# Optimization experiments

Hardware: AMD Instinct MI355X
Metric: run time of the kernel (lower is better)

The kernel has to match this reference:

```python
import jax, jax.numpy as jnp
import numpy as np

MAX_PATCH = 40   # static pad >= max points per grid cell + 1 (grid/fake token slot)
NUM_HEADS = 8


def _cumcount_1d(cell):
    """For each element, number of earlier elements with the same cell id. O(U log U) via stable sort."""
    U = cell.shape[0]
    order = jnp.argsort(cell)              # stable
    sc = cell[order]
    pos = jnp.arange(U)
    new_run = jnp.concatenate([jnp.ones((1,), bool), sc[1:] != sc[:-1]])
    run_start = jax.lax.associative_scan(jnp.maximum, jnp.where(new_run, pos, 0))  # cummax
    return jnp.zeros(U, jnp.int32).at[order].set((pos - run_start).astype(jnp.int32))


def setup_inputs() -> dict:
    key = jax.random.key(0)
    ks = jax.random.split(key, 10)
    B, U, E = 8, 8192, 256
    n = m = 32
    coords = jnp.linspace(0.0, 1.0, n)
    grid = jnp.stack(jnp.meshgrid(coords, coords, indexing='ij'), axis=-1)  # [n,m,2]
    xc_on_grid = jnp.broadcast_to(grid, (B, n, m, 2))
    xc_off_grid = jax.random.uniform(ks[0], (B, U, 2))
    zc_off_grid = jax.random.normal(ks[1], (B, U, E), jnp.float32)
    zc_on_grid = jax.random.normal(ks[2], (B, n, m, E), jnp.float32)
    latents = jax.random.normal(ks[3], (n, m, E), jnp.float32)
    fake_embedding = jax.random.normal(ks[4], (E,), jnp.float32)
    sc = 1.0 / np.sqrt(E)
    Wq = jax.random.normal(ks[5], (E, E), jnp.float32) * sc
    Wk = jax.random.normal(ks[6], (E, E), jnp.float32) * sc
    Wv = jax.random.normal(ks[7], (E, E), jnp.float32) * sc
    Wo = jax.random.normal(ks[8], (E, E), jnp.float32) * sc
    return dict(xc_off_grid=xc_off_grid, xc_on_grid=xc_on_grid,
                zc_off_grid=zc_off_grid, zc_on_grid=zc_on_grid,
                latents=latents, fake_embedding=fake_embedding,
                Wq=Wq, Wk=Wk, Wv=Wv, Wo=Wo, ignore_on_grid=0)


def reference(xc_off_grid, xc_on_grid, zc_off_grid, zc_on_grid,
              latents, fake_embedding, Wq, Wk, Wv, Wo, ignore_on_grid):
    B, U, E = zc_off_grid.shape
    _, n, m, _ = xc_on_grid.shape
    S = n * m
    MP = MAX_PATCH

    # nearest grid cell per off-grid point (uniform grid on [0,1], n points/dim)
    row = jnp.clip(jnp.round(xc_off_grid[..., 0] * (n - 1)).astype(jnp.int32), 0, n - 1)
    col = jnp.clip(jnp.round(xc_off_grid[..., 1] * (m - 1)).astype(jnp.int32), 0, m - 1)
    cell = row * m + col                                    # [B,U]

    cumcount = jax.vmap(_cumcount_1d)(cell)                 # [B,U]
    counts = jnp.zeros((B, S), jnp.int32).at[jnp.arange(B)[:, None], cell].add(1)

    # scatter off-grid tokens into padded per-cell buckets [B*S, MP, E]
    bs = (jnp.arange(B)[:, None] * S + cell).reshape(-1)
    slot = jnp.where(cumcount < MP - 1, cumcount, MP).reshape(-1)  # overflow -> dropped
    gs = jnp.zeros((B * S, MP, E), zc_off_grid.dtype)
    gs = gs.at[bs, slot].set(zc_off_grid.reshape(B * U, E), mode='drop')

    # last slot: on-grid token (or fake embedding when ignore_on_grid)
    if ignore_on_grid:
        last = jnp.broadcast_to(fake_embedding, (B * S, E))
    else:
        last = zc_on_grid.reshape(B * S, E)
    gs = gs.at[:, MP - 1].set(last)

    slots = jnp.arange(MP)
    valid = (slots[None, :] < counts.reshape(-1)[:, None]) | (slots == MP - 1)  # [B*S, MP]

    # masked MHCA: one latent query per cell attends over its bucket
    H = NUM_HEADS
    hd = E // H
    lat = jnp.broadcast_to(latents.reshape(1, S, E), (B, S, E)).reshape(B * S, E)
    q = (lat @ Wq).reshape(B * S, H, hd)
    k = (gs @ Wk).reshape(B * S, MP, H, hd)
    v = (gs @ Wv).reshape(B * S, MP, H, hd)
    scores = jnp.einsum('bhd,bphd->bhp', q, k) / np.sqrt(hd)
    scores = jnp.where(valid[:, None, :], scores, -jnp.inf)
    attn = jax.nn.softmax(scores, axis=-1)
    out = jnp.einsum('bhp,bphd->bhd', attn, v).reshape(B * S, E) @ Wo
    z_grid = out.reshape(B, n, m, E)
    return (xc_on_grid, z_grid)
```

## Files before the change

kernel.cpp:

```cpp
#include <hip/hip_runtime.h>
#include <hip/hip_bf16.h>

#define B_   8
#define U_   8192
#define E_   256
#define N_   32
#define S_   1024
#define MP_  40
#define H_   8
#define NLIST 39
#define NCAP  35
#define NTOKMAX 36
#define GCELLS (B_*S_)
#define KDIM  (H_*E_)

typedef unsigned short ushort_t;
using bf16x8 = __attribute__((ext_vector_type(8))) short;
using f32x4  = __attribute__((ext_vector_type(4))) float;

#define WS_COUNTS 0u
#define WS_LISTS  32768u
#define WS_LATB   1310720u
#define WS_WQKT   1835008u
#define WS_WVOT   2883584u
#define WS_QKB    3932160u
#define WS_W      8126464u

__device__ inline unsigned pk2(float a, float b) {
    __hip_bfloat16 x = __float2bfloat16(a), y = __float2bfloat16(b);
    return ((unsigned)(*(ushort_t*)&y) << 16) | (unsigned)(*(ushort_t*)&x);
}
__device__ inline float ubf(ushort_t u) {
    unsigned v = (unsigned)u << 16;
    return *(float*)&v;
}

__global__ __launch_bounds__(256)
void prologue(const float* __restrict__ xc_on, float* __restrict__ out,
              int* __restrict__ counts) {
    int i = blockIdx.x * 256 + threadIdx.x;
    ((float4*)out)[i] = ((const float4*)xc_on)[i];
    if (i < 2048) ((int4*)counts)[i] = make_int4(0, 0, 0, 0);
}

__global__ __launch_bounds__(256)
void mega_prep(const float* __restrict__ xc_off, const float* __restrict__ latents,
               const float* __restrict__ Wq, const float* __restrict__ Wk,
               const float* __restrict__ Wv, const float* __restrict__ Wo,
               int* __restrict__ counts, int* __restrict__ lists,
               ushort_t* __restrict__ latb, ushort_t* __restrict__ wqkT,
               ushort_t* __restrict__ wvoT) {
    __shared__ float smem[10496];
    int blk = blockIdx.x, tid = threadIdx.x;

    if (blk < 256) {
        int t = blk * 256 + tid;
        float x = xc_off[2 * t], y = xc_off[2 * t + 1];
        int row = (int)rintf(x * 31.f); row = min(max(row, 0), 31);
        int col = (int)rintf(y * 31.f); col = min(max(col, 0), 31);
        int b = t >> 13;
        int g = b * S_ + row * N_ + col;
        int old = atomicAdd(&counts[g], 1);
        if (old < NLIST) lists[g * NLIST + old] = t & (U_ - 1);
    } else if (blk < 384) {
        int i = (blk - 256) * 256 + tid;
        const float4* src = (const float4*)latents + 2 * i;
        float4 a = src[0], c = src[1];
        uint4 o;
        o.x = pk2(a.x, a.y); o.y = pk2(a.z, a.w);
        o.z = pk2(c.x, c.y); o.w = pk2(c.z, c.w);
        ((uint4*)latb)[i] = o;
    } else if (blk < 448) {
        int b2 = blk - 384, h = b2 >> 3, e0 = (b2 & 7) * 32;
        float* wq_s = smem;
        for (int i = tid; i < 8192; i += 256) {
            int f = i >> 5, d = i & 31;
            wq_s[f * 33 + d] = Wq[f * E_ + h * 32 + d];
        }
        __syncthreads();
        int e = e0 + (tid & 31), fg = tid >> 5;
        float wk[32];
        #pragma unroll
        for (int d4 = 0; d4 < 8; ++d4) {
            float4 v = *(const float4*)(Wk + (size_t)e * E_ + h * 32 + d4 * 4);
            wk[d4*4] = v.x; wk[d4*4+1] = v.y; wk[d4*4+2] = v.z; wk[d4*4+3] = v.w;
        }
        const float invs = 0.17677669529663687f;
        ushort_t* dst = wqkT + (size_t)(h * E_ + e) * E_ + fg * 32;
        for (int q8 = 0; q8 < 4; ++q8) {
            float t8[8];
            #pragma unroll
            for (int k = 0; k < 8; ++k) {
                int f = fg * 32 + q8 * 8 + k;
                float acc = 0.f;
                #pragma unroll
                for (int d = 0; d < 32; ++d) acc += wq_s[f * 33 + d] * wk[d];
                t8[k] = acc * invs;
            }
            uint4 o;
            o.x = pk2(t8[0], t8[1]); o.y = pk2(t8[2], t8[3]);
            o.z = pk2(t8[4], t8[5]); o.w = pk2(t8[6], t8[7]);
            *(uint4*)(dst + q8 * 8) = o;
        }
    } else {
        int b3 = blk - 448, h = b3 >> 2, e0p = (b3 & 3) * 64;
        float* wv_s = smem;
        float* wo_s = smem + 8448;
        for (int i = tid; i < 8192; i += 256) {
            int e = i >> 5, d = i & 31;
            wv_s[e * 33 + d] = Wv[e * E_ + h * 32 + d];
        }
        for (int i = tid; i < 2048; i += 256) {
            int d = i >> 6, el = i & 63;
            wo_s[i] = Wo[(h * 32 + d) * E_ + e0p + el];
        }
        __syncthreads();
        int erow = tid & 63, eg = tid >> 6;
        float wor[32];
        #pragma unroll
        for (int d = 0; d < 32; ++d) wor[d] = wo_s[d * 64 + erow];
        ushort_t* dst = wvoT + (size_t)(e0p + erow) * KDIM + h * E_ + eg * 64;
        for (int q8 = 0; q8 < 8; ++q8) {
            float t8[8];
            #pragma unroll
            for (int k = 0; k < 8; ++k) {
                int e = eg * 64 + q8 * 8 + k;
                float acc = 0.f;
                #pragma unroll
                for (int d = 0; d < 32; ++d) acc += wv_s[e * 33 + d] * wor[d];
                t8[k] = acc;
            }
            uint4 o;
            o.x = pk2(t8[0], t8[1]); o.y = pk2(t8[2], t8[3]);
            o.z = pk2(t8[4], t8[5]); o.w = pk2(t8[6], t8[7]);
            *(uint4*)(dst + q8 * 8) = o;
        }
    }
}

template<bool BF16OUT>
__global__ __launch_bounds__(256)
void gemm_k(const ushort_t* __restrict__ A, const ushort_t* __restrict__ BT,
            void* __restrict__ Cv, int Kdim, int Ndim, int lgNTX) {
    constexpr int LDB = 72;
    __shared__ ushort_t As[64 * LDB];
    __shared__ ushort_t Bs[64 * LDB];
    int tid = threadIdx.x;
    int idx = blockIdx.x;
    idx = (idx & 7) * (gridDim.x >> 3) + (idx >> 3);
    int nTX = 1 << lgNTX;
    int m0 = (idx >> lgNTX) * 64, n0 = (idx & (nTX - 1)) * 64;

    int wave = tid >> 6, lane = tid & 63;
    int wr = wave >> 1, wc = wave & 1;
    int l15 = lane & 15, lg = lane >> 4;

    f32x4 acc[2][2];
    #pragma unroll
    for (int m = 0; m < 2; ++m)
        #pragma unroll
        for (int n = 0; n < 2; ++n)
            acc[m][n] = (f32x4){0.f, 0.f, 0.f, 0.f};

    int r0 = tid >> 3, u0 = tid & 7;
    int r1 = r0 + 32, u1 = u0;

    const ushort_t* pa0 = A  + (size_t)(m0 + r0) * Kdim + u0 * 8;
    const ushort_t* pa1 = A  + (size_t)(m0 + r1) * Kdim + u1 * 8;
    const ushort_t* pb0 = BT + (size_t)(n0 + r0) * Kdim + u0 * 8;
    const ushort_t* pb1 = BT + (size_t)(n0 + r1) * Kdim + u1 * 8;

    uint4 a0 = *(const uint4*)(pa0);
    uint4 a1 = *(const uint4*)(pa1);
    uint4 b0 = *(const uint4*)(pb0);
    uint4 b1 = *(const uint4*)(pb1);

    for (int kt = 0; kt < Kdim; kt += 64) {
        __syncthreads();
        *(uint4*)(As + r0 * LDB + u0 * 8) = a0;
        *(uint4*)(As + r1 * LDB + u1 * 8) = a1;
        *(uint4*)(Bs + r0 * LDB + u0 * 8) = b0;
        *(uint4*)(Bs + r1 * LDB + u1 * 8) = b1;
        __syncthreads();
        if (kt + 64 < Kdim) {
            a0 = *(const uint4*)(pa0 + kt + 64);
            a1 = *(const uint4*)(pa1 + kt + 64);
            b0 = *(const uint4*)(pb0 + kt + 64);
            b1 = *(const uint4*)(pb1 + kt + 64);
        }
        #pragma unroll
        for (int kk = 0; kk < 2; ++kk) {
            bf16x8 af[2], bfr[2];
            #pragma unroll
            for (int m = 0; m < 2; ++m)
                af[m] = *(const bf16x8*)(As + (wr * 32 + m * 16 + l15) * LDB + (kk * 4 + lg) * 8);
            #pragma unroll
            for (int n = 0; n < 2; ++n)
                bfr[n] = *(const bf16x8*)(Bs + (wc * 32 + n * 16 + l15) * LDB + (kk * 4 + lg) * 8);
            #pragma unroll
            for (int m = 0; m < 2; ++m)
                #pragma unroll
                for (int n = 0; n < 2; ++n)
                    acc[m][n] = __builtin_amdgcn_mfma_f32_16x16x32_bf16(
                        af[m], bfr[n], acc[m][n], 0, 0, 0);
        }
    }
    #pragma unroll
    for (int m = 0; m < 2; ++m)
        #pragma unroll
        for (int n = 0; n < 2; ++n)
            #pragma unroll
            for (int q = 0; q < 4; ++q) {
                int row = m0 + wr * 32 + m * 16 + lg * 4 + q;
                int col = n0 + wc * 32 + n * 16 + l15;
                if (BF16OUT) {
                    __hip_bfloat16 hb = __float2bfloat16(acc[m][n][q]);
                    ((ushort_t*)Cv)[(size_t)row * Ndim + col] = *(ushort_t*)&hb;
                } else {
                    ((float*)Cv)[(size_t)row * Ndim + col] = acc[m][n][q];
                }
            }
}

__global__ __launch_bounds__(256, 8)
void pool_cells(const float* __restrict__ zc_off, const float* __restrict__ zc_on,
                const float* __restrict__ fake, const ushort_t* __restrict__ qkb,
                const int* __restrict__ counts, const int* __restrict__ lists,
                const int* __restrict__ ig_p, ushort_t* __restrict__ wout) {
    __shared__ __align__(16) ushort_t tok[NTOKMAX * E_];
    __shared__ float sc[H_ * 48];

    int g = blockIdx.x, s = g & (S_ - 1), b = g >> 10, tid = threadIdx.x;
    int h = tid >> 5, j = tid & 31;

    int cnt = min(counts[g], NCAP);
    int ntok = cnt + 1, ig = ig_p[0];
    const float* lastrow = ig ? fake : zc_on + (size_t)g * E_;

    {
        uint4* t4 = (uint4*)tok;
        for (int i = tid; i < ntok * 32; i += 256) {
            int p = i >> 5, q = i & 31;
            const float* src = (p < cnt)
                ? zc_off + ((size_t)b * U_ + lists[g * NLIST + p]) * E_
                : lastrow;
            float4 x = *(const float4*)(src + q * 8);
            float4 y = *(const float4*)(src + q * 8 + 4);
            uint4 o;
            o.x = pk2(x.x, x.y); o.y = pk2(x.z, x.w);
            o.z = pk2(y.x, y.y); o.w = pk2(y.z, y.w);
            t4[((p << 5) + q) ^ (p & 7)] = o;
        }
    }
    __syncthreads();

    if (tid < 64) {
        int l15 = tid & 15, lg = tid >> 4;
        bf16x8 af[8];
        const ushort_t* qrow = qkb + (size_t)s * KDIM + l15 * E_ + lg * 8;
        #pragma unroll
        for (int kk = 0; kk < 8; ++kk)
            af[kk] = *(const bf16x8*)(qrow + kk * 32);
        const bf16x8* tv = (const bf16x8*)tok;
        int ntiles = (ntok + 15) >> 4;
        for (int t = 0; t < ntiles; ++t) {
            f32x4 acc = (f32x4){0.f, 0.f, 0.f, 0.f};
            int row = t * 16 + l15;
            int rc = row < NTOKMAX ? row : NTOKMAX - 1;
            #pragma unroll
            for (int kk = 0; kk < 8; ++kk) {
                bf16x8 bfr = tv[((rc << 5) + (kk << 2) + lg) ^ (rc & 7)];
                acc = __builtin_amdgcn_mfma_f32_16x16x32_bf16(af[kk], bfr, acc, 0, 0, 0);
            }
            if (lg < 2) {
                #pragma unroll
                for (int q = 0; q < 4; ++q)
                    sc[(lg * 4 + q) * 48 + t * 16 + l15] = acc[q];
            }
        }
    }
    __syncthreads();

    {
        float v0 = (j < ntok) ? sc[h * 48 + j] : -1e30f;
        float v1 = (j + 32 < ntok) ? sc[h * 48 + j + 32] : -1e30f;
        float mx = fmaxf(v0, v1);
        #pragma unroll
        for (int off = 16; off; off >>= 1) mx = fmaxf(mx, __shfl_xor(mx, off, 32));
        float e0 = (j < ntok) ? __expf(v0 - mx) : 0.f;
        float e1 = (j + 32 < ntok) ? __expf(v1 - mx) : 0.f;
        float sm = e0 + e1;
        #pragma unroll
        for (int off = 16; off; off >>= 1) sm += __shfl_xor(sm, off, 32);
        float inv = 1.f / sm;
        if (j < ntok)      sc[h * 48 + j] = e0 * inv;
        if (j + 32 < ntok) sc[h * 48 + j + 32] = e1 * inv;
    }

    float acc[8];
    #pragma unroll
    for (int k = 0; k < 8; ++k) acc[k] = 0.f;
    const bf16x8* tv2 = (const bf16x8*)tok;
    for (int p = 0; p < ntok; ++p) {
        float a = sc[h * 48 + p];
        bf16x8 t8 = tv2[((p << 5) + j) ^ (p & 7)];
        #pragma unroll
        for (int k = 0; k < 8; ++k) acc[k] += a * ubf((ushort_t)t8[k]);
    }
    uint4 o;
    o.x = pk2(acc[0], acc[1]); o.y = pk2(acc[2], acc[3]);
    o.z = pk2(acc[4], acc[5]); o.w = pk2(acc[6], acc[7]);
    ((uint4*)(wout + (size_t)g * KDIM))[tid] = o;
}

extern "C" void kernel_launch(void* const* d_in, const int* in_sizes, int n_in,
                              void* d_out, int out_size, void* d_ws, size_t ws_size,
                              hipStream_t stream) {
    const float* xc_off  = (const float*)d_in[0];
    const float* xc_on   = (const float*)d_in[1];
    const float* zc_off  = (const float*)d_in[2];
    const float* zc_on   = (const float*)d_in[3];
    const float* latents = (const float*)d_in[4];
    const float* fake    = (const float*)d_in[5];
    const float* Wq      = (const float*)d_in[6];
    const float* Wk      = (const float*)d_in[7];
    const float* Wv      = (const float*)d_in[8];
    const float* Wo      = (const float*)d_in[9];
    const int*   ig      = (const int*)d_in[10];
    float* out = (float*)d_out;

    char* ws = (char*)d_ws;
    int*      counts = (int*)(ws + WS_COUNTS);
    int*      lists  = (int*)(ws + WS_LISTS);
    ushort_t* latb   = (ushort_t*)(ws + WS_LATB);
    ushort_t* wqkT   = (ushort_t*)(ws + WS_WQKT);
    ushort_t* wvoT   = (ushort_t*)(ws + WS_WVOT);
    ushort_t* qkb    = (ushort_t*)(ws + WS_QKB);
    ushort_t* w      = (ushort_t*)(ws + WS_W);

    const int PASS = B_ * N_ * N_ * 2;

    prologue<<<16, 256, 0, stream>>>(xc_on, out, counts);

    mega_prep<<<480, 256, 0, stream>>>(xc_off, latents, Wq, Wk, Wv, Wo,
                                       counts, lists, latb, wqkT, wvoT);

    gemm_k<true><<<512, 256, 0, stream>>>(latb, wqkT, qkb, 256, KDIM, 5);

    pool_cells<<<GCELLS, 256, 0, stream>>>(zc_off, zc_on, fake, qkb,
                                           counts, lists, ig, w);

    gemm_k<false><<<512, 256, 0, stream>>>(w, wvoT, out + PASS, KDIM, E_, 2);
}
```

Measured before the change: 83.57 us.

## Merge prologue into prep, fold bucket build into first GEMM, widen K tile

```diff
diff --git a/kernel.cpp b/kernel.cpp
--- a/kernel.cpp
+++ b/kernel.cpp
@@ -13,6 +13,7 @@
 #define NTOKMAX 36
 #define GCELLS (B_*S_)
 #define KDIM  (H_*E_)
+#define GEMMBLK 512
 
 typedef unsigned short ushort_t;
 using bf16x8 = __attribute__((ext_vector_type(8))) short;
@@ -36,25 +37,104 @@
 }
 
 __global__ __launch_bounds__(256)
-void prologue(const float* __restrict__ xc_on, float* __restrict__ out,
-              int* __restrict__ counts) {
-    int i = blockIdx.x * 256 + threadIdx.x;
-    ((float4*)out)[i] = ((const float4*)xc_on)[i];
-    if (i < 2048) ((int4*)counts)[i] = make_int4(0, 0, 0, 0);
-}
-
-__global__ __launch_bounds__(256)
-void mega_prep(const float* __restrict__ xc_off, const float* __restrict__ latents,
-               const float* __restrict__ Wq, const float* __restrict__ Wk,
-               const float* __restrict__ Wv, const float* __restrict__ Wo,
-               int* __restrict__ counts, int* __restrict__ lists,
-               ushort_t* __restrict__ latb, ushort_t* __restrict__ wqkT,
-               ushort_t* __restrict__ wvoT) {
+void prep(const float* __restrict__ latents,
+          const float* __restrict__ Wq, const float* __restrict__ Wk,
+          const float* __restrict__ Wv, const float* __restrict__ Wo,
+          const float* __restrict__ xc_on, float* __restrict__ out,
+          int* __restrict__ counts,
+          ushort_t* __restrict__ latb, ushort_t* __restrict__ wqkT,
+          ushort_t* __restrict__ wvoT) {
     __shared__ float smem[10496];
     int blk = blockIdx.x, tid = threadIdx.x;
 
-    if (blk < 256) {
-        int t = blk * 256 + tid;
+    if (blk < 128) {
+        int i = blk * 256 + tid;
+        const float4* src = (const float4*)latents + 2 * i;
+        float4 a = src[0], c = src[1];
+        uint4 o;
+        o.x = pk2(a.x, a.y); o.y = pk2(a.z, a.w);
+        o.z = pk2(c.x, c.y); o.w = pk2(c.z, c.w);
+        ((uint4*)latb)[i] = o;
+    } else if (blk < 192) {
+        int b2 = blk - 128, h = b2 >> 3, e0 = (b2 & 7) * 32;
+        float* wq_s = smem;
+        for (int i = tid; i < 8192; i += 256) {
+            int f = i >> 5, d = i & 31;
+            wq_s[f * 33 + d] = Wq[f * E_ + h * 32 + d];
+        }
+        __syncthreads();
+        int e = e0 + (tid & 31), fg = tid >> 5;
+        float wk[32];
+        #pragma unroll
+        for (int d4 = 0; d4 < 8; ++d4) {
+            float4 v = *(const float4*)(Wk + (size_t)e * E_ + h * 32 + d4 * 4);
+            wk[d4*4] = v.x; wk[d4*4+1] = v.y; wk[d4*4+2] = v.z; wk[d4*4+3] = v.w;
+        }
+        const float invs = 0.17677669529663687f;
+        ushort_t* dst = wqkT + (size_t)(h * E_ + e) * E_ + fg * 32;
+        for (int q8 = 0; q8 < 4; ++q8) {
+            float t8[8];
+            #pragma unroll
+            for (int k = 0; k < 8; ++k) {
+                int f = fg * 32 + q8 * 8 + k;
+                float acc = 0.f;
+                #pragma unroll
+                for (int d = 0; d < 32; ++d) acc += wq_s[f * 33 + d] * wk[d];
+                t8[k] = acc * invs;
+            }
+            uint4 o;
+            o.x = pk2(t8[0], t8[1]); o.y = pk2(t8[2], t8[3]);
+            o.z = pk2(t8[4], t8[5]); o.w = pk2(t8[6], t8[7]);
+            *(uint4*)(dst + q8 * 8) = o;
+        }
+    } else if (blk < 224) {
+        int b3 = blk - 192, h = b3 >> 2, e0p = (b3 & 3) * 64;
+        float* wv_s = smem;
+        float* wo_s = smem + 8448;
+        for (int i = tid; i < 8192; i += 256) {
+            int e = i >> 5, d = i & 31;
+            wv_s[e * 33 + d] = Wv[e * E_ + h * 32 + d];
+        }
+        for (int i = tid; i < 2048; i += 256) {
+            int d = i >> 6, el = i & 63;
+            wo_s[i] = Wo[(h * 32 + d) * E_ + e0p + el];
+        }
+        __syncthreads();
+        int erow = tid & 63, eg = tid >> 6;
+        float wor[32];
+        #pragma unroll
+        for (int d = 0; d < 32; ++d) wor[d] = wo_s[d * 64 + erow];
+        ushort_t* dst = wvoT + (size_t)(e0p + erow) * KDIM + h * E_ + eg * 64;
+        for (int q8 = 0; q8 < 8; ++q8) {
+            float t8[8];
+            #pragma unroll
+            for (int k = 0; k < 8; ++k) {
+                int e = eg * 64 + q8 * 8 + k;
+                float acc = 0.f;
+                #pragma unroll
+                for (int d = 0; d < 32; ++d) acc += wv_s[e * 33 + d] * wor[d];
+                t8[k] = acc;
+            }
+            uint4 o;
+            o.x = pk2(t8[0], t8[1]); o.y = pk2(t8[2], t8[3]);
+            o.z = pk2(t8[4], t8[5]); o.w = pk2(t8[6], t8[7]);
+            *(uint4*)(dst + q8 * 8) = o;
+        }
+    } else {
+        int i = (blk - 224) * 256 + tid;
+        ((float4*)out)[i] = ((const float4*)xc_on)[i];
+        if (i < 2048) ((int4*)counts)[i] = make_int4(0, 0, 0, 0);
+    }
+}
+
+template<int BKT, bool BF16OUT, bool DO_BUILD>
+__global__ __launch_bounds__(256)
+void gemm_k(const ushort_t* __restrict__ A, const ushort_t* __restrict__ BT,
+            void* __restrict__ Cv, int Kdim, int Ndim, int lgNTX,
+            const float* __restrict__ xc_off, int* __restrict__ counts,
+            int* __restrict__ lists) {
+    if (DO_BUILD && (int)blockIdx.x >= GEMMBLK) {
+        int t = ((int)blockIdx.x - GEMMBLK) * 256 + threadIdx.x;
         float x = xc_off[2 * t], y = xc_off[2 * t + 1];
         int row = (int)rintf(x * 31.f); row = min(max(row, 0), 31);
         int col = (int)rintf(y * 31.f); col = min(max(col, 0), 31);
@@ -62,92 +142,16 @@
         int g = b * S_ + row * N_ + col;
         int old = atomicAdd(&counts[g], 1);
         if (old < NLIST) lists[g * NLIST + old] = t & (U_ - 1);
-    } else if (blk < 384) {
-        int i = (blk - 256) * 256 + tid;
-        const float4* src = (const float4*)latents + 2 * i;
-        float4 a = src[0], c = src[1];
-        uint4 o;
-        o.x = pk2(a.x, a.y); o.y = pk2(a.z, a.w);
-        o.z = pk2(c.x, c.y); o.w = pk2(c.z, c.w);
-        ((uint4*)latb)[i] = o;
-    } else if (blk < 448) {
-        int b2 = blk - 384, h = b2 >> 3, e0 = (b2 & 7) * 32;
-        float* wq_s = smem;
-        for (int i = tid; i < 8192; i += 256) {
-            int f = i >> 5, d = i & 31;
-            wq_s[f * 33 + d] = Wq[f * E_ + h * 32 + d];
-        }
-        __syncthreads();
-        int e = e0 + (tid & 31), fg = tid >> 5;
-        float wk[32];
-        #pragma unroll
-        for (int d4 = 0; d4 < 8; ++d4) {
-            float4 v = *(const float4*)(Wk + (size_t)e * E_ + h * 32 + d4 * 4);
-            wk[d4*4] = v.x; wk[d4*4+1] = v.y; wk[d4*4+2] = v.z; wk[d4*4+3] = v.w;
-        }
-        const float invs = 0.17677669529663687f;
-        ushort_t* dst = wqkT + (size_t)(h * E_ + e) * E_ + fg * 32;
-        for (int q8 = 0; q8 < 4; ++q8) {
-            float t8[8];
-            #pragma unroll
-            for (int k = 0; k < 8; ++k) {
-                int f = fg * 32 + q8 * 8 + k;
-                float acc = 0.f;
-                #pragma unroll
-                for (int d = 0; d < 32; ++d) acc += wq_s[f * 33 + d] * wk[d];
-                t8[k] = acc * invs;
-            }
-            uint4 o;
-            o.x = pk2(t8[0], t8[1]); o.y = pk2(t8[2], t8[3]);
-            o.z = pk2(t8[4], t8[5]); o.w = pk2(t8[6], t8[7]);
-            *(uint4*)(dst + q8 * 8) = o;
-        }
-    } else {
-        int b3 = blk - 448, h = b3 >> 2, e0p = (b3 & 3) * 64;
-        float* wv_s = smem;
-        float* wo_s = smem + 8448;
-        for (int i = tid; i < 8192; i += 256) {
-            int e = i >> 5, d = i & 31;
-            wv_s[e * 33 + d] = Wv[e * E_ + h * 32 + d];
-        }
-        for (int i = tid; i < 2048; i += 256) {
-            int d = i >> 6, el = i & 63;
-            wo_s[i] = Wo[(h * 32 + d) * E_ + e0p + el];
-        }
-        __syncthreads();
-        int erow = tid & 63, eg = tid >> 6;
-        float wor[32];
-        #pragma unroll
-        for (int d = 0; d < 32; ++d) wor[d] = wo_s[d * 64 + erow];
-        ushort_t* dst = wvoT + (size_t)(e0p + erow) * KDIM + h * E_ + eg * 64;
-        for (int q8 = 0; q8 < 8; ++q8) {
-            float t8[8];
-            #pragma unroll
-            for (int k = 0; k < 8; ++k) {
-                int e = eg * 64 + q8 * 8 + k;
-                float acc = 0.f;
-                #pragma unroll
-                for (int d = 0; d < 32; ++d) acc += wv_s[e * 33 + d] * wor[d];
-                t8[k] = acc;
-            }
-            uint4 o;
-            o.x = pk2(t8[0], t8[1]); o.y = pk2(t8[2], t8[3]);
-            o.z = pk2(t8[4], t8[5]); o.w = pk2(t8[6], t8[7]);
-            *(uint4*)(dst + q8 * 8) = o;
-        }
-    }
-}
-
-template<bool BF16OUT>
-__global__ __launch_bounds__(256)
-void gemm_k(const ushort_t* __restrict__ A, const ushort_t* __restrict__ BT,
-            void* __restrict__ Cv, int Kdim, int Ndim, int lgNTX) {
-    constexpr int LDB = 72;
+        return;
+    }
+    constexpr int LDB = BKT + 8;
+    constexpr int SPR = BKT / 8;
+    constexpr int PT  = 64 * SPR / 256;
     __shared__ ushort_t As[64 * LDB];
     __shared__ ushort_t Bs[64 * LDB];
     int tid = threadIdx.x;
     int idx = blockIdx.x;
-    idx = (idx & 7) * (gridDim.x >> 3) + (idx >> 3);
+    idx = (idx & 7) * (GEMMBLK >> 3) + (idx >> 3);
     int nTX = 1 << lgNTX;
     int m0 = (idx >> lgNTX) * 64, n0 = (idx & (nTX - 1)) * 64;
 
@@ -162,34 +166,34 @@
         for (int n = 0; n < 2; ++n)
             acc[m][n] = (f32x4){0.f, 0.f, 0.f, 0.f};
 
-    int r0 = tid >> 3, u0 = tid & 7;
-    int r1 = r0 + 32, u1 = u0;
-
-    const ushort_t* pa0 = A  + (size_t)(m0 + r0) * Kdim + u0 * 8;
-    const ushort_t* pa1 = A  + (size_t)(m0 + r1) * Kdim + u1 * 8;
-    const ushort_t* pb0 = BT + (size_t)(n0 + r0) * Kdim + u0 * 8;
-    const ushort_t* pb1 = BT + (size_t)(n0 + r1) * Kdim + u1 * 8;
-
-    uint4 a0 = *(const uint4*)(pa0);
-    uint4 a1 = *(const uint4*)(pa1);
-    uint4 b0 = *(const uint4*)(pb0);
-    uint4 b1 = *(const uint4*)(pb1);
-
-    for (int kt = 0; kt < Kdim; kt += 64) {
+    int rr = tid / SPR, uu = tid % SPR;
+    const ushort_t* pa = A  + (size_t)(m0 + rr) * Kdim + uu * 8;
+    const ushort_t* pb = BT + (size_t)(n0 + rr) * Kdim + uu * 8;
+
+    uint4 ar[PT], br[PT];
+    #pragma unroll
+    for (int i = 0; i < PT; ++i) {
+        ar[i] = *(const uint4*)(pa + (size_t)i * 16 * Kdim);
+        br[i] = *(const uint4*)(pb + (size_t)i * 16 * Kdim);
+    }
+
+    for (int kt = 0; kt < Kdim; kt += BKT) {
         __syncthreads();
-        *(uint4*)(As + r0 * LDB + u0 * 8) = a0;
-        *(uint4*)(As + r1 * LDB + u1 * 8) = a1;
-        *(uint4*)(Bs + r0 * LDB + u0 * 8) = b0;
-        *(uint4*)(Bs + r1 * LDB + u1 * 8) = b1;
+        #pragma unroll
+        for (int i = 0; i < PT; ++i) {
+            *(uint4*)(As + (rr + i * 16) * LDB + uu * 8) = ar[i];
+            *(uint4*)(Bs + (rr + i * 16) * LDB + uu * 8) = br[i];
+        }
         __syncthreads();
-        if (kt + 64 < Kdim) {
-            a0 = *(const uint4*)(pa0 + kt + 64);
-            a1 = *(const uint4*)(pa1 + kt + 64);
-            b0 = *(const uint4*)(pb0 + kt + 64);
-            b1 = *(const uint4*)(pb1 + kt + 64);
-        }
-        #pragma unroll
-        for (int kk = 0; kk < 2; ++kk) {
+        if (kt + BKT < Kdim) {
+            #pragma unroll
+            for (int i = 0; i < PT; ++i) {
+                ar[i] = *(const uint4*)(pa + (size_t)i * 16 * Kdim + kt + BKT);
+                br[i] = *(const uint4*)(pb + (size_t)i * 16 * Kdim + kt + BKT);
+            }
+        }
+        #pragma unroll
+        for (int kk = 0; kk < BKT / 32; ++kk) {
             bf16x8 af[2], bfr[2];
             #pragma unroll
             for (int m = 0; m < 2; ++m)
@@ -340,15 +344,15 @@
 
     const int PASS = B_ * N_ * N_ * 2;
 
-    prologue<<<16, 256, 0, stream>>>(xc_on, out, counts);
-
-    mega_prep<<<480, 256, 0, stream>>>(xc_off, latents, Wq, Wk, Wv, Wo,
-                                       counts, lists, latb, wqkT, wvoT);
-
-    gemm_k<true><<<512, 256, 0, stream>>>(latb, wqkT, qkb, 256, KDIM, 5);
+    prep<<<240, 256, 0, stream>>>(latents, Wq, Wk, Wv, Wo, xc_on, out,
+                                  counts, latb, wqkT, wvoT);
+
+    gemm_k<128, true, true><<<GEMMBLK + 256, 256, 0, stream>>>(
+        latb, wqkT, qkb, 256, KDIM, 5, xc_off, counts, lists);
 
     pool_cells<<<GCELLS, 256, 0, stream>>>(zc_off, zc_on, fake, qkb,
                                            counts, lists, ig, w);
 
-    gemm_k<false><<<512, 256, 0, stream>>>(w, wvoT, out + PASS, KDIM, E_, 2);
-}
+    gemm_k<128, false, false><<<GEMMBLK, 256, 0, stream>>>(
+        w, wvoT, out + PASS, KDIM, E_, 2, nullptr, nullptr, nullptr);
+}
```

New measurement: 138.2 us. 1.65x slower.
